# Kernel tuning notes

Measured on AMD Instinct MI355X. Metric: run time of the kernel, lower is better.

The kernel has to match this reference:

```python
import jax, jax.numpy as jnp
import numpy as np

B, S, S2, H, NH, DF, NL, NLAYER = 512, 6, 32, 256, 8, 2048, 3, 3
HD = H // NH


def _layernorm(x, g, b, eps=1e-5):
    mu = x.mean(-1, keepdims=True)
    var = ((x - mu) ** 2).mean(-1, keepdims=True)
    return (x - mu) / jnp.sqrt(var + eps) * g + b


def _pos_encoding(seq, d):
    pos = jnp.arange(seq, dtype=jnp.float32)[:, None]
    div = jnp.exp(jnp.arange(0, d, 2, dtype=jnp.float32) * (-jnp.log(10000.0) / d))
    ang = pos * div  # [seq, d/2]
    return jnp.stack([jnp.sin(ang), jnp.cos(ang)], axis=-1).reshape(seq, d)


def setup_inputs() -> dict:
    key = jax.random.key(0)
    ks = iter(jax.random.split(key, 40))
    sc = 0.02
    inp = {}
    inp['states'] = jax.random.normal(next(ks), (B, S, H), jnp.float32)
    inp['state_mask'] = jax.random.randint(next(ks), (B, S), 0, 2).astype(jnp.float32)
    inp['actions'] = jax.random.normal(next(ks), (B, S2, H), jnp.float32)
    inp['actions_mask'] = jnp.ones((B, S2), jnp.float32)
    # TransformerEncoder params (3 layers, stacked on leading axis)
    inp['Wqkv'] = jax.random.normal(next(ks), (NLAYER, 3 * H, H), jnp.float32) * sc
    inp['bqkv'] = jnp.zeros((NLAYER, 3 * H), jnp.float32)
    inp['Wo'] = jax.random.normal(next(ks), (NLAYER, H, H), jnp.float32) * sc
    inp['bo'] = jnp.zeros((NLAYER, H), jnp.float32)
    inp['ln1_g'] = jnp.ones((NLAYER, H), jnp.float32)
    inp['ln1_b'] = jnp.zeros((NLAYER, H), jnp.float32)
    inp['W1'] = jax.random.normal(next(ks), (NLAYER, DF, H), jnp.float32) * sc
    inp['b1'] = jnp.zeros((NLAYER, DF), jnp.float32)
    inp['W2'] = jax.random.normal(next(ks), (NLAYER, H, DF), jnp.float32) * sc
    inp['b2'] = jnp.zeros((NLAYER, H), jnp.float32)
    inp['ln2_g'] = jnp.ones((NLAYER, H), jnp.float32)
    inp['ln2_b'] = jnp.zeros((NLAYER, H), jnp.float32)
    # attn_layer MLP: Linear(2H->H), ReLU, Linear(H->1), ReLU
    inp['Wa1'] = jax.random.normal(next(ks), (H, 2 * H), jnp.float32) * sc
    inp['ba1'] = jnp.zeros((H,), jnp.float32)
    inp['Wa2'] = jax.random.normal(next(ks), (1, H), jnp.float32) * sc
    inp['ba2'] = jnp.zeros((1,), jnp.float32)
    # dueling value head
    inp['Wv'] = jax.random.normal(next(ks), (1, H), jnp.float32) * sc
    inp['bv'] = jnp.zeros((1,), jnp.float32)
    # per-label bilinear weight [num_labels, H, H] + bias
    inp['Wlab'] = jax.random.normal(next(ks), (NL, H, H), jnp.float32) * sc
    inp['blab'] = jax.random.normal(next(ks), (NL,), jnp.float32) * sc
    return inp


def _forward(states, state_mask, actions, actions_mask, Wqkv, bqkv, Wo, bo,
             ln1_g, ln1_b, W1, b1, W2, b2, ln2_g, ln2_b,
             Wa1, ba1, Wa2, ba2, Wv, bv, Wlab, blab):
    batch, seq, hs = states.shape
    seq2 = actions.shape[1]
    # positional encoding along seq axis (eval mode: dropout = identity)
    x = states + _pos_encoding(seq, hs)[None, :, :]
    # Faithful to original: [batch, seq, h] is fed to a seq-first torch
    # TransformerEncoder, so self-attention mixes across the BATCH axis (L=batch,
    # N=seq). Post-LN layers, relu FFN, dim_feedforward=2048.
    for i in range(NLAYER):
        L, N = x.shape[0], x.shape[1]
        qkv = jnp.einsum('lne,fe->lnf', x, Wqkv[i]) + bqkv[i]
        q, k, v = jnp.split(qkv, 3, axis=-1)
        q = q.reshape(L, N, NH, HD)
        k = k.reshape(L, N, NH, HD)
        v = v.reshape(L, N, NH, HD)
        scores = jnp.einsum('lnhd,mnhd->nhlm', q, k) / jnp.sqrt(jnp.float32(HD))
        attn = jax.nn.softmax(scores, axis=-1)
        ctx = jnp.einsum('nhlm,mnhd->lnhd', attn, v).reshape(L, N, hs)
        sa = jnp.einsum('lne,fe->lnf', ctx, Wo[i]) + bo[i]
        x = _layernorm(x + sa, ln1_g[i], ln1_b[i])
        hmid = jax.nn.relu(jnp.einsum('lne,fe->lnf', x, W1[i]) + b1[i])
        ff = jnp.einsum('lnf,ef->lne', hmid, W2[i]) + b2[i]
        x = _layernorm(x + ff, ln2_g[i], ln2_b[i])
    out = x  # [batch, seq, h]
    # --- attention_aggregate(actions, out, out, actions_mask, state_mask) ---
    mask = actions_mask[:, :, None] * state_mask[:, None, :]  # [B, seq2, seq]
    stack = jnp.concatenate([
        jnp.broadcast_to(actions[:, :, None, :], (batch, seq2, seq, hs)),
        jnp.broadcast_to(out[:, None, :, :], (batch, seq2, seq, hs)),
    ], axis=-1)  # [B, seq2, seq, 2H]
    h1 = jax.nn.relu(jnp.einsum('bqkf,hf->bqkh', stack, Wa1) + ba1)
    a = jax.nn.relu(jnp.einsum('bqkh,oh->bqko', h1, Wa2)[..., 0] + ba2[0])
    A = jnp.where(mask > 0, jnp.exp(a), 0.0)  # masked_fill(-inf).exp()
    attn_w = A / jnp.clip(A.sum(-1, keepdims=True), 2e-15, None)
    states_feat = jnp.einsum('bqk,bkh->bqh', attn_w, out)  # [B, seq2, H]
    # -------------------------------------------------------------------
    actions_num = actions_mask.sum(1)[:, None, None]  # [B,1,1]
    states_feat_mean = states_feat.sum(1, keepdims=True) / actions_num  # [B,1,H]
    # adv[b,s,l] = sum_ij actions[b,s,i] * Wlab[l,i,j] * states_feat[b,s,j] + blab[l]
    adv = jnp.einsum('bsi,lij,bsj->bsl', actions, Wlab, states_feat) + blab
    val = states_feat_mean @ Wv.T + bv  # [B,1,1]
    q_value = val + adv - adv.mean(axis=(1, 2), keepdims=True)  # [B, seq2, NL]
    # actions_mask is all-ones -> no_pad selection keeps every row
    return q_value.reshape(-1, NL)


def reference(states, state_mask, actions, actions_mask, Wqkv, bqkv, Wo, bo,
              ln1_g, ln1_b, W1, b1, W2, b2, ln2_g, ln2_b,
              Wa1, ba1, Wa2, ba2, Wv, bv, Wlab, blab):
    return _forward(states, state_mask, actions, actions_mask, Wqkv, bqkv, Wo, bo,
                    ln1_g, ln1_b, W1, b1, W2, b2, ln2_g, ln2_b,
                    Wa1, ba1, Wa2, ba2, Wv, bv, Wlab, blab)
```

## Files before the change

kernel.cpp:

```cpp
#include <hip/hip_runtime.h>

using u16 = unsigned short;
typedef __attribute__((ext_vector_type(8))) short bf16x8;
typedef __attribute__((ext_vector_type(4))) float f32x4;

__device__ __forceinline__ float b2f(u16 u) { return __uint_as_float(((unsigned)u) << 16); }
__device__ __forceinline__ u16 f2b(float f) {
  unsigned x = __float_as_uint(f);
  return (u16)((x + 0x7FFFu + ((x >> 16) & 1u)) >> 16);
}

__device__ __align__(16) float g_xf[786432];
__device__ __align__(16) u16   g_xb[786432];
__device__ __align__(16) u16   g_qkv[2359296];
__device__ __align__(16) u16   g_ctx[786432];
__device__ __align__(16) u16   g_hmid[6291456];
__device__ __align__(16) u16   g_wb[3932160];
__device__ __align__(16) u16   g_actb[4194304];
__device__ __align__(16) u16   g_wa1b[131072];
__device__ __align__(16) u16   g_wlabb[196608];
__device__ __align__(16) float g_par[344584];
__device__ __align__(16) float g_Pa[4194304];
__device__ __align__(16) float g_Po[786432];
__device__ __align__(16) u16   g_sfb[4194304];
__device__ float g_val[512];
__device__ float g_adv[49152];

#define OFF_BQKV 0
#define OFF_BO   2304
#define OFF_B1   3072
#define OFF_B2   9216
#define OFF_LN1G 9984
#define OFF_LN1B 10752
#define OFF_LN2G 11520
#define OFF_LN2B 12288
#define OFF_BA1  144128
#define OFF_WA2  144384
#define OFF_WV   144640
#define OFF_BLAB 341504
#define OFF_BA2  341508
#define OFF_BV   341509
#define OFF_MASK 341512

#define LP 40

__device__ __forceinline__ int get_flag(const unsigned* ln1g) {
  return (ln1g[0] == 0x3F800000u) ? 0 : 1;
}

struct PJob { const void* src; void* dst; void* dst2; int n; int kind; };
struct PJobs { PJob e[23]; };
__global__ __launch_bounds__(256) void prep_kernel(PJobs jobs, const unsigned* __restrict__ ln1g) {
  PJob j = jobs.e[blockIdx.y];
  int fl = get_flag(ln1g);
  int stride = gridDim.x * 256;
  int i0 = blockIdx.x * 256 + threadIdx.x;
  if (j.kind == 0) {
    float* dst = (float*)j.dst;
    for (int i = i0; i < j.n; i += stride)
      dst[i] = fl ? b2f(((const u16*)j.src)[i]) : ((const float*)j.src)[i];
  } else if (j.kind == 1) {
    int n8 = j.n >> 3;
    uint4* d = (uint4*)j.dst;
    if (fl) {
      const uint4* s = (const uint4*)j.src;
      for (int i = i0; i < n8; i += stride) d[i] = s[i];
    } else {
      const f32x4* s = (const f32x4*)j.src;
      for (int i = i0; i < n8; i += stride) {
        f32x4 v0 = s[i * 2];
        f32x4 v1 = s[i * 2 + 1];
        u16 tmp[8];
        #pragma unroll
        for (int k = 0; k < 4; k++) { tmp[k] = f2b(v0[k]); tmp[4 + k] = f2b(v1[k]); }
        d[i] = *(const uint4*)tmp;
      }
    }
  } else {
    float* xf = (float*)j.dst;
    u16* xb = (u16*)j.dst2;
    const float c = -9.210340371976184f / 256.f;
    for (int i = i0; i < j.n; i += stride) {
      size_t base = (size_t)i * 4;
      int t = (int)(base >> 8);
      int e = (int)(base & 255);
      int n = t % 6;
      int half = e >> 1;
      float dv0 = expf((float)(2 * half) * c);
      float dv1 = expf((float)(2 * (half + 1)) * c);
      float a0 = (float)n * dv0, a1 = (float)n * dv1;
      f32x4 p = { sinf(a0), cosf(a0), sinf(a1), cosf(a1) };
      f32x4 s;
      if (fl) {
        ushort4 u = *(const ushort4*)((const u16*)j.src + base);
        s[0] = b2f(u.x); s[1] = b2f(u.y); s[2] = b2f(u.z); s[3] = b2f(u.w);
      } else {
        s = *(const f32x4*)((const float*)j.src + base);
      }
      f32x4 v;
      #pragma unroll
      for (int k = 0; k < 4; k++) v[k] = s[k] + p[k];
      *(f32x4*)(xf + base) = v;
      ushort4 ob = { f2b(v[0]), f2b(v[1]), f2b(v[2]), f2b(v[3]) };
      *(ushort4*)(xb + base) = ob;
    }
  }
}

__device__ __forceinline__ float block_sum(float v, float* red) {
  int lane = threadIdx.x & 63;
  int w = threadIdx.x >> 6;
  #pragma unroll
  for (int o = 32; o > 0; o >>= 1) v += __shfl_down(v, o, 64);
  __syncthreads();
  if (lane == 0) red[w] = v;
  __syncthreads();
  int nw = blockDim.x >> 6;
  float s = 0.f;
  for (int i = 0; i < nw; i++) s += red[i];
  return s;
}

template <typename TC, bool RELU>
__global__ __launch_bounds__(256) void mfma_gemm(const u16* __restrict__ A,
                                                 const u16* __restrict__ B,
                                                 const float* __restrict__ bias,
                                                 TC* __restrict__ C,
                                                 int K, int lda, int ldb, int ldc) {
  __shared__ __align__(16) short As[64 * LP];
  __shared__ __align__(16) short Bs[64 * LP];
  int tx = threadIdx.x;
  int row0 = blockIdx.y * 64, col0 = blockIdx.x * 64;
  int lr = tx >> 2, lc = (tx & 3) * 8;
  int lane = tx & 63, w = tx >> 6;
  int wr = (w >> 1) * 32, wc = (w & 1) * 32;
  int q = lane >> 4, mr = lane & 15;
  f32x4 acc[2][2] = {};
  const short* Ap = (const short*)A;
  const short* Bp = (const short*)B;
  for (int k0 = 0; k0 < K; k0 += 32) {
    uint4 av = *(const uint4*)(Ap + (size_t)(row0 + lr) * lda + k0 + lc);
    uint4 bv = *(const uint4*)(Bp + (size_t)(col0 + lr) * ldb + k0 + lc);
    __syncthreads();
    *(uint4*)(As + lr * LP + lc) = av;
    *(uint4*)(Bs + lr * LP + lc) = bv;
    __syncthreads();
    bf16x8 af0 = *(const bf16x8*)(As + (wr + mr) * LP + q * 8);
    bf16x8 af1 = *(const bf16x8*)(As + (wr + 16 + mr) * LP + q * 8);
    bf16x8 bf0 = *(const bf16x8*)(Bs + (wc + mr) * LP + q * 8);
    bf16x8 bf1 = *(const bf16x8*)(Bs + (wc + 16 + mr) * LP + q * 8);
    acc[0][0] = __builtin_amdgcn_mfma_f32_16x16x32_bf16(af0, bf0, acc[0][0], 0, 0, 0);
    acc[0][1] = __builtin_amdgcn_mfma_f32_16x16x32_bf16(af0, bf1, acc[0][1], 0, 0, 0);
    acc[1][0] = __builtin_amdgcn_mfma_f32_16x16x32_bf16(af1, bf0, acc[1][0], 0, 0, 0);
    acc[1][1] = __builtin_amdgcn_mfma_f32_16x16x32_bf16(af1, bf1, acc[1][1], 0, 0, 0);
  }
  #pragma unroll
  for (int j = 0; j < 2; j++) {
    int col = col0 + wc + j * 16 + mr;
    float bv_ = bias ? bias[col] : 0.f;
    #pragma unroll
    for (int i = 0; i < 2; i++) {
      #pragma unroll
      for (int r = 0; r < 4; r++) {
        int row = row0 + wr + i * 16 + q * 4 + r;
        float v = acc[i][j][r] + bv_;
        if (RELU) v = fmaxf(v, 0.f);
        if constexpr (sizeof(TC) == 4) C[(size_t)row * ldc + col] = v;
        else C[(size_t)row * ldc + col] = f2b(v);
      }
    }
  }
}

template <typename TC, bool RELU>
__global__ __launch_bounds__(256) void mfma_gemm128(const u16* __restrict__ A,
                                                    const u16* __restrict__ B,
                                                    const float* __restrict__ bias,
                                                    TC* __restrict__ C,
                                                    int K, int lda, int ldb, int ldc) {
  __shared__ __align__(16) short As[128 * LP];
  __shared__ __align__(16) short Bs[128 * LP];
  int tx = threadIdx.x;
  int row0 = blockIdx.y * 128, col0 = blockIdx.x * 128;
  int lr = tx >> 2, lc = (tx & 3) * 8;
  int lane = tx & 63, w = tx >> 6;
  int wr = (w >> 1) * 64, wc = (w & 1) * 64;
  int q = lane >> 4, mr = lane & 15;
  f32x4 acc[4][4] = {};
  const short* Ap = (const short*)A;
  const short* Bp = (const short*)B;
  for (int k0 = 0; k0 < K; k0 += 32) {
    uint4 a0 = *(const uint4*)(Ap + (size_t)(row0 + lr) * lda + k0 + lc);
    uint4 a1 = *(const uint4*)(Ap + (size_t)(row0 + 64 + lr) * lda + k0 + lc);
    uint4 b0 = *(const uint4*)(Bp + (size_t)(col0 + lr) * ldb + k0 + lc);
    uint4 b1 = *(const uint4*)(Bp + (size_t)(col0 + 64 + lr) * ldb + k0 + lc);
    __syncthreads();
    *(uint4*)(As + lr * LP + lc) = a0;
    *(uint4*)(As + (64 + lr) * LP + lc) = a1;
    *(uint4*)(Bs + lr * LP + lc) = b0;
    *(uint4*)(Bs + (64 + lr) * LP + lc) = b1;
    __syncthreads();
    bf16x8 af[4], bf[4];
    #pragma unroll
    for (int i = 0; i < 4; i++) af[i] = *(const bf16x8*)(As + (wr + i * 16 + mr) * LP + q * 8);
    #pragma unroll
    for (int j = 0; j < 4; j++) bf[j] = *(const bf16x8*)(Bs + (wc + j * 16 + mr) * LP + q * 8);
    #pragma unroll
    for (int i = 0; i < 4; i++)
      #pragma unroll
      for (int j = 0; j < 4; j++)
        acc[i][j] = __builtin_amdgcn_mfma_f32_16x16x32_bf16(af[i], bf[j], acc[i][j], 0, 0, 0);
  }
  #pragma unroll
  for (int j = 0; j < 4; j++) {
    int col = col0 + wc + j * 16 + mr;
    float bv_ = bias ? bias[col] : 0.f;
    #pragma unroll
    for (int i = 0; i < 4; i++) {
      #pragma unroll
      for (int r = 0; r < 4; r++) {
        int row = row0 + wr + i * 16 + q * 4 + r;
        float v = acc[i][j][r] + bv_;
        if (RELU) v = fmaxf(v, 0.f);
        if constexpr (sizeof(TC) == 4) C[(size_t)row * ldc + col] = v;
        else C[(size_t)row * ldc + col] = f2b(v);
      }
    }
  }
}

__global__ __launch_bounds__(256) void mfma_gemm_adv(const u16* __restrict__ A,
                                                     const u16* __restrict__ B,
                                                     const u16* __restrict__ actb,
                                                     float* __restrict__ adv,
                                                     int K, int lda, int ldb) {
  __shared__ __align__(16) short As[128 * LP];
  __shared__ __align__(16) short Bs[128 * LP];
  int tx = threadIdx.x;
  int row0 = blockIdx.y * 128, col0 = blockIdx.x * 128;
  int lr = tx >> 2, lc = (tx & 3) * 8;
  int lane = tx & 63, w = tx >> 6;
  int wr = (w >> 1) * 64, wc = (w & 1) * 64;
  int q = lane >> 4, mr = lane & 15;
  f32x4 acc[4][4] = {};
  const short* Ap = (const short*)A;
  const short* Bp = (const short*)B;
  for (int k0 = 0; k0 < K; k0 += 32) {
    uint4 a0 = *(const uint4*)(Ap + (size_t)(row0 + lr) * lda + k0 + lc);
    uint4 a1 = *(const uint4*)(Ap + (size_t)(row0 + 64 + lr) * lda + k0 + lc);
    uint4 b0 = *(const uint4*)(Bp + (size_t)(col0 + lr) * ldb + k0 + lc);
    uint4 b1 = *(const uint4*)(Bp + (size_t)(col0 + 64 + lr) * ldb + k0 + lc);
    __syncthreads();
    *(uint4*)(As + lr * LP + lc) = a0;
    *(uint4*)(As + (64 + lr) * LP + lc) = a1;
    *(uint4*)(Bs + lr * LP + lc) = b0;
    *(uint4*)(Bs + (64 + lr) * LP + lc) = b1;
    __syncthreads();
    bf16x8 af[4], bf[4];
    #pragma unroll
    for (int i = 0; i < 4; i++) af[i] = *(const bf16x8*)(As + (wr + i * 16 + mr) * LP + q * 8);
    #pragma unroll
    for (int j = 0; j < 4; j++) bf[j] = *(const bf16x8*)(Bs + (wc + j * 16 + mr) * LP + q * 8);
    #pragma unroll
    for (int i = 0; i < 4; i++)
      #pragma unroll
      for (int j = 0; j < 4; j++)
        acc[i][j] = __builtin_amdgcn_mfma_f32_16x16x32_bf16(af[i], bf[j], acc[i][j], 0, 0, 0);
  }
  int l = (col0 + wc) >> 8;
  #pragma unroll
  for (int i = 0; i < 4; i++) {
    #pragma unroll
    for (int r = 0; r < 4; r++) {
      int row = row0 + wr + i * 16 + q * 4 + r;
      float s = 0.f;
      #pragma unroll
      for (int j = 0; j < 4; j++) {
        int icol = (col0 + wc + j * 16 + mr) & 255;
        s += acc[i][j][r] * b2f(actb[(size_t)row * 256 + icol]);
      }
      s += __shfl_xor(s, 1, 64);
      s += __shfl_xor(s, 2, 64);
      s += __shfl_xor(s, 4, 64);
      s += __shfl_xor(s, 8, 64);
      if (mr == 0) atomicAdd(&adv[(size_t)row * 3 + l], s);
    }
  }
}

#define LP64 72
template <typename TC, bool RELU>
__global__ __launch_bounds__(256) void mfma_gemm_bk64(const u16* __restrict__ A,
                                                      const u16* __restrict__ B,
                                                      const float* __restrict__ bias,
                                                      TC* __restrict__ C,
                                                      int K, int lda, int ldb, int ldc) {
  __shared__ __align__(16) short As[64 * LP64];
  __shared__ __align__(16) short Bs[64 * LP64];
  int tx = threadIdx.x;
  int row0 = blockIdx.y * 64, col0 = blockIdx.x * 64;
  int lr = tx >> 2, lc = (tx & 3) * 16;
  int lane = tx & 63, w = tx >> 6;
  int wr = (w >> 1) * 32, wc = (w & 1) * 32;
  int q = lane >> 4, mr = lane & 15;
  f32x4 acc[2][2] = {};
  const short* Ap = (const short*)A;
  const short* Bp = (const short*)B;
  for (int k0 = 0; k0 < K; k0 += 64) {
    uint4 a0 = *(const uint4*)(Ap + (size_t)(row0 + lr) * lda + k0 + lc);
    uint4 a1 = *(const uint4*)(Ap + (size_t)(row0 + lr) * lda + k0 + lc + 8);
    uint4 b0 = *(const uint4*)(Bp + (size_t)(col0 + lr) * ldb + k0 + lc);
    uint4 b1 = *(const uint4*)(Bp + (size_t)(col0 + lr) * ldb + k0 + lc + 8);
    __syncthreads();
    *(uint4*)(As + lr * LP64 + lc) = a0;
    *(uint4*)(As + lr * LP64 + lc + 8) = a1;
    *(uint4*)(Bs + lr * LP64 + lc) = b0;
    *(uint4*)(Bs + lr * LP64 + lc + 8) = b1;
    __syncthreads();
    #pragma unroll
    for (int kk = 0; kk < 64; kk += 32) {
      bf16x8 af0 = *(const bf16x8*)(As + (wr + mr) * LP64 + kk + q * 8);
      bf16x8 af1 = *(const bf16x8*)(As + (wr + 16 + mr) * LP64 + kk + q * 8);
      bf16x8 bf0 = *(const bf16x8*)(Bs + (wc + mr) * LP64 + kk + q * 8);
      bf16x8 bf1 = *(const bf16x8*)(Bs + (wc + 16 + mr) * LP64 + kk + q * 8);
      acc[0][0] = __builtin_amdgcn_mfma_f32_16x16x32_bf16(af0, bf0, acc[0][0], 0, 0, 0);
      acc[0][1] = __builtin_amdgcn_mfma_f32_16x16x32_bf16(af0, bf1, acc[0][1], 0, 0, 0);
      acc[1][0] = __builtin_amdgcn_mfma_f32_16x16x32_bf16(af1, bf0, acc[1][0], 0, 0, 0);
      acc[1][1] = __builtin_amdgcn_mfma_f32_16x16x32_bf16(af1, bf1, acc[1][1], 0, 0, 0);
    }
  }
  #pragma unroll
  for (int j = 0; j < 2; j++) {
    int col = col0 + wc + j * 16 + mr;
    float bv_ = bias ? bias[col] : 0.f;
    #pragma unroll
    for (int i = 0; i < 2; i++) {
      #pragma unroll
      for (int r = 0; r < 4; r++) {
        int row = row0 + wr + i * 16 + q * 4 + r;
        float v = acc[i][j][r] + bv_;
        if (RELU) v = fmaxf(v, 0.f);
        if constexpr (sizeof(TC) == 4) C[(size_t)row * ldc + col] = v;
        else C[(size_t)row * ldc + col] = f2b(v);
      }
    }
  }
}

__global__ __launch_bounds__(256) void attn_mfma(const u16* __restrict__ qkv,
                                                 u16* __restrict__ ctx) {
  __shared__ __align__(16) u16 VT[32 * 72];
  __shared__ __align__(16) u16 Ss[64 * 72];
  int tx = threadIdx.x;
  int w = tx >> 6, lane = tx & 63;
  int q = lane >> 4, mr = lane & 15;
  int nh = blockIdx.y;
  int n = nh >> 3, h = nh & 7;
  int l0 = blockIdx.x * 64;
  int lrow = l0 + w * 16 + mr;
  bf16x8 af = *(const bf16x8*)(qkv + ((size_t)lrow * 6 + n) * 768 + h * 32 + q * 8);
  const float scale = 0.17677669529663687f;
  f32x4 acc_o[2] = {};
  float dpart[4] = {0.f, 0.f, 0.f, 0.f};
  for (int mi = 0; mi < 8; mi++) {
    int m0 = mi * 64;
    __syncthreads();
    {
      int row = tx >> 2;
      int dc = (tx & 3) * 8;
      uint4 vv = *(const uint4*)(qkv + ((size_t)(m0 + row) * 6 + n) * 768 + 512 + h * 32 + dc);
      u16 tmp[8];
      *(uint4*)tmp = vv;
      #pragma unroll
      for (int i = 0; i < 8; i++) VT[(dc + i) * 72 + row] = tmp[i];
    }
    f32x4 accs[4];
    #pragma unroll
    for (int nt = 0; nt < 4; nt++) {
      bf16x8 bf = *(const bf16x8*)(qkv + ((size_t)(m0 + nt * 16 + mr) * 6 + n) * 768 +
                                   256 + h * 32 + q * 8);
      f32x4 z = {0.f, 0.f, 0.f, 0.f};
      accs[nt] = __builtin_amdgcn_mfma_f32_16x16x32_bf16(af, bf, z, 0, 0, 0);
    }
    #pragma unroll
    for (int nt = 0; nt < 4; nt++) {
      #pragma unroll
      for (int r = 0; r < 4; r++) {
        float e = __expf(fminf(accs[nt][r] * scale, 60.f));
        dpart[r] += e;
        Ss[(w * 16 + q * 4 + r) * 72 + nt * 16 + mr] = f2b(e);
      }
    }
    __syncthreads();
    #pragma unroll
    for (int dt = 0; dt < 2; dt++) {
      #pragma unroll
      for (int kc = 0; kc < 2; kc++) {
        bf16x8 ap = *(const bf16x8*)(Ss + (w * 16 + mr) * 72 + kc * 32 + q * 8);
        bf16x8 bv = *(const bf16x8*)(VT + (dt * 16 + mr) * 72 + kc * 32 + q * 8);
        acc_o[dt] = __builtin_amdgcn_mfma_f32_16x16x32_bf16(ap, bv, acc_o[dt], 0, 0, 0);
      }
    }
  }
  #pragma unroll
  for (int r = 0; r < 4; r++) {
    float d = dpart[r];
    d += __shfl_xor(d, 1, 64);
    d += __shfl_xor(d, 2, 64);
    d += __shfl_xor(d, 4, 64);
    d += __shfl_xor(d, 8, 64);
    dpart[r] = d;
  }
  #pragma unroll
  for (int dt = 0; dt < 2; dt++) {
    #pragma unroll
    for (int r = 0; r < 4; r++) {
      int l = l0 + w * 16 + q * 4 + r;
      int d = dt * 16 + mr;
      ctx[((size_t)l * 6 + n) * 256 + h * 32 + d] = f2b(acc_o[dt][r] / dpart[r]);
    }
  }
}

__global__ __launch_bounds__(256) void ln_kernel(float* __restrict__ xf,
                                                 u16* __restrict__ xb,
                                                 const u16* __restrict__ addend,
                                                 const float* __restrict__ g,
                                                 const float* __restrict__ b) {
  int row = blockIdx.x * 4 + (threadIdx.x >> 6);
  int lane = threadIdx.x & 63;
  size_t base = (size_t)row * 256 + lane * 4;
  f32x4 x = *(const f32x4*)(xf + base);
  ushort4 ad = *(const ushort4*)(addend + base);
  f32x4 v;
  v[0] = x[0] + b2f(ad.x); v[1] = x[1] + b2f(ad.y);
  v[2] = x[2] + b2f(ad.z); v[3] = x[3] + b2f(ad.w);
  float s = (v[0] + v[1]) + (v[2] + v[3]);
  #pragma unroll
  for (int o = 32; o > 0; o >>= 1) s += __shfl_xor(s, o, 64);
  float mu = s * (1.f / 256.f);
  f32x4 d;
  #pragma unroll
  for (int j = 0; j < 4; j++) d[j] = v[j] - mu;
  float s2 = (d[0] * d[0] + d[1] * d[1]) + (d[2] * d[2] + d[3] * d[3]);
  #pragma unroll
  for (int o = 32; o > 0; o >>= 1) s2 += __shfl_xor(s2, o, 64);
  float rstd = 1.f / sqrtf(s2 * (1.f / 256.f) + 1e-5f);
  f32x4 gg = *(const f32x4*)(g + lane * 4);
  f32x4 bb = *(const f32x4*)(b + lane * 4);
  f32x4 y;
  #pragma unroll
  for (int j = 0; j < 4; j++) y[j] = d[j] * rstd * gg[j] + bb[j];
  *(f32x4*)(xf + base) = y;
  ushort4 ob = { f2b(y[0]), f2b(y[1]), f2b(y[2]), f2b(y[3]) };
  *(ushort4*)(xb + base) = ob;
}

#define PAP 260
__global__ __launch_bounds__(256) void agg_val_kernel(const float* __restrict__ Pa,
                                                      const float* __restrict__ Po,
                                                      const float* __restrict__ Wa2,
                                                      const float* __restrict__ ba2,
                                                      const float* __restrict__ state_mask,
                                                      const float* __restrict__ out,
                                                      const float* __restrict__ Wv,
                                                      const float* __restrict__ bv,
                                                      u16* __restrict__ sfb,
                                                      float* __restrict__ val,
                                                      float* __restrict__ adv) {
  __shared__ __align__(16) float Pa_s[32 * PAP];
  __shared__ __align__(16) float Po_s[6 * PAP];
  __shared__ __align__(16) float out_s[6 * 256];
  __shared__ __align__(16) float wa2_s[256];
  __shared__ float Aw_s[192];
  __shared__ float inv_den_s[32];
  __shared__ float red[4];
  int b = blockIdx.x;
  int tx = threadIdx.x;
  if (tx < 96) adv[(size_t)b * 96 + tx] = 0.f;
  #pragma unroll
  for (int i = tx; i < 2048; i += 256) {
    int r = i >> 6, c4 = (i & 63) * 4;
    f32x4 v = *(const f32x4*)(Pa + ((size_t)(b * 32 + r) * 256 + c4));
    *(f32x4*)(Pa_s + r * PAP + c4) = v;
  }
  if (tx < 128) {
    int r = tx >> 6, c4 = (tx & 63) * 4;
    f32x4 v0 = *(const f32x4*)(Po + ((size_t)(b * 6 + r) * 256 + c4));
    f32x4 v1 = *(const f32x4*)(Po + ((size_t)(b * 6 + r + 2) * 256 + c4));
    f32x4 v2 = *(const f32x4*)(Po + ((size_t)(b * 6 + r + 4) * 256 + c4));
    *(f32x4*)(Po_s + r * PAP + c4) = v0;
    *(f32x4*)(Po_s + (r + 2) * PAP + c4) = v1;
    *(f32x4*)(Po_s + (r + 4) * PAP + c4) = v2;
  } else {
    int i = tx - 128;
    #pragma unroll
    for (int j = 0; j < 3; j++) {
      int e4 = (i + j * 128) * 4;
      f32x4 v = *(const f32x4*)(out + (size_t)b * 1536 + e4);
      *(f32x4*)(out_s + e4) = v;
    }
  }
  if (tx < 64) *(f32x4*)(wa2_s + tx * 4) = *(const f32x4*)(Wa2 + tx * 4);
  __syncthreads();
  if (tx < 192) {
    int q = tx / 6, k = tx - q * 6;
    const float* paP = Pa_s + q * PAP;
    const float* poP = Po_s + k * PAP;
    float a0 = 0.f, a1 = 0.f, a2 = 0.f, a3 = 0.f;
    #pragma unroll 4
    for (int h = 0; h < 256; h += 4) {
      f32x4 pa = *(const f32x4*)(paP + h);
      f32x4 po = *(const f32x4*)(poP + h);
      f32x4 wv = *(const f32x4*)(wa2_s + h);
      a0 += fmaxf(pa[0] + po[0], 0.f) * wv[0];
      a1 += fmaxf(pa[1] + po[1], 0.f) * wv[1];
      a2 += fmaxf(pa[2] + po[2], 0.f) * wv[2];
      a3 += fmaxf(pa[3] + po[3], 0.f) * wv[3];
    }
    float s = (a0 + a1) + (a2 + a3) + ba2[0];
    float a = fminf(fmaxf(s, 0.f), 80.f);
    Aw_s[tx] = (state_mask[b * 6 + k] > 0.f) ? __expf(a) : 0.f;
  }
  __syncthreads();
  if (tx < 32) {
    const float* aw = Aw_s + tx * 6;
    float d = ((aw[0] + aw[1]) + (aw[2] + aw[3])) + (aw[4] + aw[5]);
    inv_den_s[tx] = 1.f / fmaxf(d, 2e-15f);
  }
  __syncthreads();
  float o0 = out_s[tx], o1 = out_s[256 + tx], o2 = out_s[512 + tx];
  float o3 = out_s[768 + tx], o4 = out_s[1024 + tx], o5 = out_s[1280 + tx];
  float msum = 0.f;
  #pragma unroll 4
  for (int q = 0; q < 32; q++) {
    const float* aw = Aw_s + q * 6;
    float acc = aw[0] * o0 + aw[1] * o1 + aw[2] * o2 + aw[3] * o3 + aw[4] * o4 + aw[5] * o5;
    float sfv = acc * inv_den_s[q];
    sfb[((size_t)(b * 32 + q)) * 256 + tx] = f2b(sfv);
    msum += sfv;
  }
  float vc = msum * (1.f / 32.f) * Wv[tx];
  float tot = block_sum(vc, red);
  if (tx == 0) val[b] = tot + bv[0];
}

__global__ __launch_bounds__(128) void final_kernel(const float* __restrict__ adv,
                                                    const float* __restrict__ blab,
                                                    const float* __restrict__ val,
                                                    void* __restrict__ out,
                                                    const unsigned* __restrict__ ln1g) {
  int b = blockIdx.x, t = threadIdx.x;
  __shared__ float red[2];
  float v = (t < 96) ? adv[(size_t)b * 96 + t] + blab[t % 3] : 0.f;
  float s = block_sum(v, red);
  float mean = s * (1.f / 96.f);
  if (t < 96) {
    float q = val[b] + v - mean;
    if (get_flag(ln1g)) ((u16*)out)[(size_t)b * 96 + t] = f2b(q);
    else                ((float*)out)[(size_t)b * 96 + t] = q;
  }
}

extern "C" void kernel_launch(void* const* d_in, const int* in_sizes, int n_in,
                              void* d_out, int out_size, void* d_ws, size_t ws_size,
                              hipStream_t stream) {
  float *xf, *par, *Pa, *Po, *val, *adv;
  u16 *xb, *qkvb, *ctxb, *hmidb, *wb, *actb, *wa1b, *wlabb, *sfb;
  hipGetSymbolAddress((void**)&xf,    HIP_SYMBOL(g_xf));
  hipGetSymbolAddress((void**)&xb,    HIP_SYMBOL(g_xb));
  hipGetSymbolAddress((void**)&qkvb,  HIP_SYMBOL(g_qkv));
  hipGetSymbolAddress((void**)&ctxb,  HIP_SYMBOL(g_ctx));
  hipGetSymbolAddress((void**)&hmidb, HIP_SYMBOL(g_hmid));
  hipGetSymbolAddress((void**)&wb,    HIP_SYMBOL(g_wb));
  hipGetSymbolAddress((void**)&actb,  HIP_SYMBOL(g_actb));
  hipGetSymbolAddress((void**)&wa1b,  HIP_SYMBOL(g_wa1b));
  hipGetSymbolAddress((void**)&wlabb, HIP_SYMBOL(g_wlabb));
  hipGetSymbolAddress((void**)&par,   HIP_SYMBOL(g_par));
  hipGetSymbolAddress((void**)&Pa,    HIP_SYMBOL(g_Pa));
  hipGetSymbolAddress((void**)&Po,    HIP_SYMBOL(g_Po));
  hipGetSymbolAddress((void**)&sfb,   HIP_SYMBOL(g_sfb));
  hipGetSymbolAddress((void**)&val,   HIP_SYMBOL(g_val));
  hipGetSymbolAddress((void**)&adv,   HIP_SYMBOL(g_adv));
  const unsigned* ln1g = (const unsigned*)d_in[8];
  u16* sab = hmidb;
  u16* ffb = ctxb;

  PJobs pj;
  pj.e[0]  = { d_in[5],  par + OFF_BQKV, nullptr, 2304, 0 };
  pj.e[1]  = { d_in[7],  par + OFF_BO,   nullptr, 768,  0 };
  pj.e[2]  = { d_in[11], par + OFF_B1,   nullptr, 6144, 0 };
  pj.e[3]  = { d_in[13], par + OFF_B2,   nullptr, 768,  0 };
  pj.e[4]  = { d_in[8],  par + OFF_LN1G, nullptr, 768,  0 };
  pj.e[5]  = { d_in[9],  par + OFF_LN1B, nullptr, 768,  0 };
  pj.e[6]  = { d_in[14], par + OFF_LN2G, nullptr, 768,  0 };
  pj.e[7]  = { d_in[15], par + OFF_LN2B, nullptr, 768,  0 };
  pj.e[8]  = { d_in[17], par + OFF_BA1,  nullptr, 256,  0 };
  pj.e[9]  = { d_in[18], par + OFF_WA2,  nullptr, 256,  0 };
  pj.e[10] = { d_in[20], par + OFF_WV,   nullptr, 256,  0 };
  pj.e[11] = { d_in[23], par + OFF_BLAB, nullptr, 3,    0 };
  pj.e[12] = { d_in[19], par + OFF_BA2,  nullptr, 1,    0 };
  pj.e[13] = { d_in[21], par + OFF_BV,   nullptr, 1,    0 };
  pj.e[14] = { d_in[1],  par + OFF_MASK, nullptr, 3072, 0 };
  pj.e[15] = { d_in[4],  wb,             nullptr, 589824,  1 };
  pj.e[16] = { d_in[6],  wb + 589824,    nullptr, 196608,  1 };
  pj.e[17] = { d_in[10], wb + 786432,    nullptr, 1572864, 1 };
  pj.e[18] = { d_in[12], wb + 2359296,   nullptr, 1572864, 1 };
  pj.e[19] = { d_in[16], wa1b,           nullptr, 131072,  1 };
  pj.e[20] = { d_in[22], wlabb,          nullptr, 196608,  1 };
  pj.e[21] = { d_in[2],  actb,           nullptr, 4194304, 1 };
  pj.e[22] = { d_in[0],  xf,             xb,      196608,  2 };
  prep_kernel<<<dim3(128, 23), 256, 0, stream>>>(pj, ln1g);

  for (int i = 0; i < 3; i++) {
    mfma_gemm128<u16, false><<<dim3(6, 24), 256, 0, stream>>>(
        xb, wb + (size_t)i * 196608, par + OFF_BQKV + i * 768, qkvb, 256, 256, 256, 768);
    attn_mfma<<<dim3(8, 48), 256, 0, stream>>>(qkvb, ctxb);
    mfma_gemm<u16, false><<<dim3(4, 48), 256, 0, stream>>>(
        ctxb, wb + 589824 + (size_t)i * 65536, par + OFF_BO + i * 256, sab, 256, 256, 256, 256);
    ln_kernel<<<768, 256, 0, stream>>>(xf, xb, sab, par + OFF_LN1G + i * 256, par + OFF_LN1B + i * 256);
    mfma_gemm128<u16, true><<<dim3(16, 24), 256, 0, stream>>>(
        xb, wb + 786432 + (size_t)i * 524288, par + OFF_B1 + i * 2048, hmidb, 256, 256, 256, 2048);
    mfma_gemm_bk64<u16, false><<<dim3(4, 48), 256, 0, stream>>>(
        hmidb, wb + 2359296 + (size_t)i * 524288, par + OFF_B2 + i * 256, ffb, 2048, 2048, 2048, 256);
    ln_kernel<<<768, 256, 0, stream>>>(xf, xb, ffb, par + OFF_LN2G + i * 256, par + OFF_LN2B + i * 256);
  }

  mfma_gemm128<float, false><<<dim3(2, 128), 256, 0, stream>>>(
      actb, wa1b, par + OFF_BA1, Pa, 256, 256, 512, 256);
  mfma_gemm<float, false><<<dim3(4, 48), 256, 0, stream>>>(
      xb, wa1b + 256, nullptr, Po, 256, 256, 512, 256);

  agg_val_kernel<<<512, 256, 0, stream>>>(Pa, Po, par + OFF_WA2, par + OFF_BA2,
                                          par + OFF_MASK, xf, par + OFF_WV,
                                          par + OFF_BV, sfb, val, adv);

  mfma_gemm_adv<<<dim3(6, 128), 256, 0, stream>>>(sfb, wlabb, actb, adv, 256, 256, 256);
  final_kernel<<<512, 128, 0, stream>>>(adv, par + OFF_BLAB, val, d_out, ln1g);
}
```

Baseline: 286.9 us.

## Store attention MLP projections in bf16, fuse Pa/Po GEMMs, retile QKV and W2 GEMMs

Merges the two attention-MLP projection GEMMs into a single launch and stores their outputs as bf16 instead of fp32, halving intermediate traffic into agg_val_kernel. Replaces the W2 GEMM with a 64x32 output tile so twice as many blocks run in parallel, and moves the QKV projection from the 128-tile GEMM to the smaller-tile GEMM for more blocks. The bf16 storage of Pa/Po adds rounding before the ReLU/attention-score stage, which slightly changes numerics.

```diff
diff --git a/kernel.cpp b/kernel.cpp
--- a/kernel.cpp
+++ b/kernel.cpp
@@ -20,8 +20,8 @@
 __device__ __align__(16) u16   g_wa1b[131072];
 __device__ __align__(16) u16   g_wlabb[196608];
 __device__ __align__(16) float g_par[344584];
-__device__ __align__(16) float g_Pa[4194304];
-__device__ __align__(16) float g_Po[786432];
+__device__ __align__(16) u16   g_Pab[4194304];
+__device__ __align__(16) u16   g_Pob[786432];
 __device__ __align__(16) u16   g_sfb[4194304];
 __device__ float g_val[512];
 __device__ float g_adv[49152];
@@ -229,6 +229,71 @@
   }
 }
 
+__global__ __launch_bounds__(256) void papo_kernel(const u16* __restrict__ actb,
+                                                   const u16* __restrict__ xb,
+                                                   const u16* __restrict__ wa1b,
+                                                   const float* __restrict__ ba1,
+                                                   u16* __restrict__ Pab,
+                                                   u16* __restrict__ Pob) {
+  __shared__ __align__(16) short As[128 * LP];
+  __shared__ __align__(16) short Bs[128 * LP];
+  const short* Ap;
+  const short* Bp;
+  const float* bias;
+  u16* C;
+  int row0;
+  if (blockIdx.y < 128) {
+    Ap = (const short*)actb; Bp = (const short*)wa1b; bias = ba1; C = Pab;
+    row0 = blockIdx.y * 128;
+  } else {
+    Ap = (const short*)xb; Bp = (const short*)(wa1b + 256); bias = nullptr; C = Pob;
+    row0 = (blockIdx.y - 128) * 128;
+  }
+  const int K = 256, lda = 256, ldb = 512, ldc = 256;
+  int tx = threadIdx.x;
+  int col0 = blockIdx.x * 128;
+  int lr = tx >> 2, lc = (tx & 3) * 8;
+  int lane = tx & 63, w = tx >> 6;
+  int wr = (w >> 1) * 64, wc = (w & 1) * 64;
+  int q = lane >> 4, mr = lane & 15;
+  f32x4 acc[4][4] = {};
+  for (int k0 = 0; k0 < K; k0 += 32) {
+    uint4 a0 = *(const uint4*)(Ap + (size_t)(row0 + lr) * lda + k0 + lc);
+    uint4 a1 = *(const uint4*)(Ap + (size_t)(row0 + 64 + lr) * lda + k0 + lc);
+    uint4 b0 = *(const uint4*)(Bp + (size_t)(col0 + lr) * ldb + k0 + lc);
+    uint4 b1 = *(const uint4*)(Bp + (size_t)(col0 + 64 + lr) * ldb + k0 + lc);
+    __syncthreads();
+    *(uint4*)(As + lr * LP + lc) = a0;
+    *(uint4*)(As + (64 + lr) * LP + lc) = a1;
+    *(uint4*)(Bs + lr * LP + lc) = b0;
+    *(uint4*)(Bs + (64 + lr) * LP + lc) = b1;
+    __syncthreads();
+    bf16x8 af[4], bf[4];
+    #pragma unroll
+    for (int i = 0; i < 4; i++) af[i] = *(const bf16x8*)(As + (wr + i * 16 + mr) * LP + q * 8);
+    #pragma unroll
+    for (int j = 0; j < 4; j++) bf[j] = *(const bf16x8*)(Bs + (wc + j * 16 + mr) * LP + q * 8);
+    #pragma unroll
+    for (int i = 0; i < 4; i++)
+      #pragma unroll
+      for (int j = 0; j < 4; j++)
+        acc[i][j] = __builtin_amdgcn_mfma_f32_16x16x32_bf16(af[i], bf[j], acc[i][j], 0, 0, 0);
+  }
+  #pragma unroll
+  for (int j = 0; j < 4; j++) {
+    int col = col0 + wc + j * 16 + mr;
+    float bv_ = bias ? bias[col] : 0.f;
+    #pragma unroll
+    for (int i = 0; i < 4; i++) {
+      #pragma unroll
+      for (int r = 0; r < 4; r++) {
+        int row = row0 + wr + i * 16 + q * 4 + r;
+        C[(size_t)row * ldc + col] = f2b(acc[i][j][r] + bv_);
+      }
+    }
+  }
+}
+
 __global__ __launch_bounds__(256) void mfma_gemm_adv(const u16* __restrict__ A,
                                                      const u16* __restrict__ B,
                                                      const u16* __restrict__ actb,
@@ -289,60 +354,49 @@
 }
 
 #define LP64 72
-template <typename TC, bool RELU>
-__global__ __launch_bounds__(256) void mfma_gemm_bk64(const u16* __restrict__ A,
-                                                      const u16* __restrict__ B,
-                                                      const float* __restrict__ bias,
-                                                      TC* __restrict__ C,
-                                                      int K, int lda, int ldb, int ldc) {
+__global__ __launch_bounds__(256) void mfma_gemm_w2(const u16* __restrict__ A,
+                                                    const u16* __restrict__ B,
+                                                    const float* __restrict__ bias,
+                                                    u16* __restrict__ C,
+                                                    int K, int lda, int ldb, int ldc) {
   __shared__ __align__(16) short As[64 * LP64];
-  __shared__ __align__(16) short Bs[64 * LP64];
+  __shared__ __align__(16) short Bs[32 * LP64];
   int tx = threadIdx.x;
-  int row0 = blockIdx.y * 64, col0 = blockIdx.x * 64;
-  int lr = tx >> 2, lc = (tx & 3) * 16;
+  int row0 = blockIdx.y * 64, col0 = blockIdx.x * 32;
   int lane = tx & 63, w = tx >> 6;
-  int wr = (w >> 1) * 32, wc = (w & 1) * 32;
+  int wr = (w >> 1) * 32, wc = (w & 1) * 16;
   int q = lane >> 4, mr = lane & 15;
-  f32x4 acc[2][2] = {};
+  int alr = tx >> 2, alc = (tx & 3) * 16;
+  int blr = tx >> 3, blc = (tx & 7) * 8;
+  f32x4 acc[2] = {};
   const short* Ap = (const short*)A;
   const short* Bp = (const short*)B;
   for (int k0 = 0; k0 < K; k0 += 64) {
-    uint4 a0 = *(const uint4*)(Ap + (size_t)(row0 + lr) * lda + k0 + lc);
-    uint4 a1 = *(const uint4*)(Ap + (size_t)(row0 + lr) * lda + k0 + lc + 8);
-    uint4 b0 = *(const uint4*)(Bp + (size_t)(col0 + lr) * ldb + k0 + lc);
-    uint4 b1 = *(const uint4*)(Bp + (size_t)(col0 + lr) * ldb + k0 + lc + 8);
-    __syncthreads();
-    *(uint4*)(As + lr * LP64 + lc) = a0;
-    *(uint4*)(As + lr * LP64 + lc + 8) = a1;
-    *(uint4*)(Bs + lr * LP64 + lc) = b0;
-    *(uint4*)(Bs + lr * LP64 + lc + 8) = b1;
+    uint4 a0 = *(const uint4*)(Ap + (size_t)(row0 + alr) * lda + k0 + alc);
+    uint4 a1 = *(const uint4*)(Ap + (size_t)(row0 + alr) * lda + k0 + alc + 8);
+    uint4 b0 = *(const uint4*)(Bp + (size_t)(col0 + blr) * ldb + k0 + blc);
+    __syncthreads();
+    *(uint4*)(As + alr * LP64 + alc) = a0;
+    *(uint4*)(As + alr * LP64 + alc + 8) = a1;
+    *(uint4*)(Bs + blr * LP64 + blc) = b0;
     __syncthreads();
     #pragma unroll
     for (int kk = 0; kk < 64; kk += 32) {
       bf16x8 af0 = *(const bf16x8*)(As + (wr + mr) * LP64 + kk + q * 8);
       bf16x8 af1 = *(const bf16x8*)(As + (wr + 16 + mr) * LP64 + kk + q * 8);
-      bf16x8 bf0 = *(const bf16x8*)(Bs + (wc + mr) * LP64 + kk + q * 8);
-      bf16x8 bf1 = *(const bf16x8*)(Bs + (wc + 16 + mr) * LP64 + kk + q * 8);
-      acc[0][0] = __builtin_amdgcn_mfma_f32_16x16x32_bf16(af0, bf0, acc[0][0], 0, 0, 0);
-      acc[0][1] = __builtin_amdgcn_mfma_f32_16x16x32_bf16(af0, bf1, acc[0][1], 0, 0, 0);
-      acc[1][0] = __builtin_amdgcn_mfma_f32_16x16x32_bf16(af1, bf0, acc[1][0], 0, 0, 0);
-      acc[1][1] = __builtin_amdgcn_mfma_f32_16x16x32_bf16(af1, bf1, acc[1][1], 0, 0, 0);
-    }
-  }
-  #pragma unroll
-  for (int j = 0; j < 2; j++) {
-    int col = col0 + wc + j * 16 + mr;
-    float bv_ = bias ? bias[col] : 0.f;
-    #pragma unroll
-    for (int i = 0; i < 2; i++) {
-      #pragma unroll
-      for (int r = 0; r < 4; r++) {
-        int row = row0 + wr + i * 16 + q * 4 + r;
-        float v = acc[i][j][r] + bv_;
-        if (RELU) v = fmaxf(v, 0.f);
-        if constexpr (sizeof(TC) == 4) C[(size_t)row * ldc + col] = v;
-        else C[(size_t)row * ldc + col] = f2b(v);
-      }
+      bf16x8 bf = *(const bf16x8*)(Bs + (wc + mr) * LP64 + kk + q * 8);
+      acc[0] = __builtin_amdgcn_mfma_f32_16x16x32_bf16(af0, bf, acc[0], 0, 0, 0);
+      acc[1] = __builtin_amdgcn_mfma_f32_16x16x32_bf16(af1, bf, acc[1], 0, 0, 0);
+    }
+  }
+  int col = col0 + wc + mr;
+  float bv_ = bias ? bias[col] : 0.f;
+  #pragma unroll
+  for (int i = 0; i < 2; i++) {
+    #pragma unroll
+    for (int r = 0; r < 4; r++) {
+      int row = row0 + wr + i * 16 + q * 4 + r;
+      C[(size_t)row * ldc + col] = f2b(acc[i][r] + bv_);
     }
   }
 }
@@ -457,8 +511,8 @@
 }
 
 #define PAP 260
-__global__ __launch_bounds__(256) void agg_val_kernel(const float* __restrict__ Pa,
-                                                      const float* __restrict__ Po,
+__global__ __launch_bounds__(256) void agg_val_kernel(const u16* __restrict__ Pab,
+                                                      const u16* __restrict__ Pob,
                                                       const float* __restrict__ Wa2,
                                                       const float* __restrict__ ba2,
                                                       const float* __restrict__ state_mask,
@@ -479,27 +533,23 @@
   int tx = threadIdx.x;
   if (tx < 96) adv[(size_t)b * 96 + tx] = 0.f;
   #pragma unroll
-  for (int i = tx; i < 2048; i += 256) {
-    int r = i >> 6, c4 = (i & 63) * 4;
-    f32x4 v = *(const f32x4*)(Pa + ((size_t)(b * 32 + r) * 256 + c4));
-    *(f32x4*)(Pa_s + r * PAP + c4) = v;
-  }
-  if (tx < 128) {
-    int r = tx >> 6, c4 = (tx & 63) * 4;
-    f32x4 v0 = *(const f32x4*)(Po + ((size_t)(b * 6 + r) * 256 + c4));
-    f32x4 v1 = *(const f32x4*)(Po + ((size_t)(b * 6 + r + 2) * 256 + c4));
-    f32x4 v2 = *(const f32x4*)(Po + ((size_t)(b * 6 + r + 4) * 256 + c4));
-    *(f32x4*)(Po_s + r * PAP + c4) = v0;
-    *(f32x4*)(Po_s + (r + 2) * PAP + c4) = v1;
-    *(f32x4*)(Po_s + (r + 4) * PAP + c4) = v2;
-  } else {
-    int i = tx - 128;
-    #pragma unroll
-    for (int j = 0; j < 3; j++) {
-      int e4 = (i + j * 128) * 4;
-      f32x4 v = *(const f32x4*)(out + (size_t)b * 1536 + e4);
-      *(f32x4*)(out_s + e4) = v;
-    }
+  for (int i = tx; i < 1024; i += 256) {
+    int r = i >> 5, c8 = (i & 31) * 8;
+    u16 vv[8];
+    *(uint4*)vv = *(const uint4*)(Pab + ((size_t)(b * 32 + r) * 256 + c8));
+    #pragma unroll
+    for (int k = 0; k < 8; k++) Pa_s[r * PAP + c8 + k] = b2f(vv[k]);
+  }
+  if (tx < 192) {
+    int r = tx >> 5, c8 = (tx & 31) * 8;
+    u16 vv[8];
+    *(uint4*)vv = *(const uint4*)(Pob + ((size_t)(b * 6 + r) * 256 + c8));
+    #pragma unroll
+    for (int k = 0; k < 8; k++) Po_s[r * PAP + c8 + k] = b2f(vv[k]);
+  }
+  for (int i = tx; i < 384; i += 256) {
+    int e4 = i * 4;
+    *(f32x4*)(out_s + e4) = *(const f32x4*)(out + (size_t)b * 1536 + e4);
   }
   if (tx < 64) *(f32x4*)(wa2_s + tx * 4) = *(const f32x4*)(Wa2 + tx * 4);
   __syncthreads();
@@ -565,8 +615,8 @@
 extern "C" void kernel_launch(void* const* d_in, const int* in_sizes, int n_in,
                               void* d_out, int out_size, void* d_ws, size_t ws_size,
                               hipStream_t stream) {
-  float *xf, *par, *Pa, *Po, *val, *adv;
-  u16 *xb, *qkvb, *ctxb, *hmidb, *wb, *actb, *wa1b, *wlabb, *sfb;
+  float *xf, *par, *val, *adv;
+  u16 *xb, *qkvb, *ctxb, *hmidb, *wb, *actb, *wa1b, *wlabb, *sfb, *Pab, *Pob;
   hipGetSymbolAddress((void**)&xf,    HIP_SYMBOL(g_xf));
   hipGetSymbolAddress((void**)&xb,    HIP_SYMBOL(g_xb));
   hipGetSymbolAddress((void**)&qkvb,  HIP_SYMBOL(g_qkv));
@@ -577,8 +627,8 @@
   hipGetSymbolAddress((void**)&wa1b,  HIP_SYMBOL(g_wa1b));
   hipGetSymbolAddress((void**)&wlabb, HIP_SYMBOL(g_wlabb));
   hipGetSymbolAddress((void**)&par,   HIP_SYMBOL(g_par));
-  hipGetSymbolAddress((void**)&Pa,    HIP_SYMBOL(g_Pa));
-  hipGetSymbolAddress((void**)&Po,    HIP_SYMBOL(g_Po));
+  hipGetSymbolAddress((void**)&Pab,   HIP_SYMBOL(g_Pab));
+  hipGetSymbolAddress((void**)&Pob,   HIP_SYMBOL(g_Pob));
   hipGetSymbolAddress((void**)&sfb,   HIP_SYMBOL(g_sfb));
   hipGetSymbolAddress((void**)&val,   HIP_SYMBOL(g_val));
   hipGetSymbolAddress((void**)&adv,   HIP_SYMBOL(g_adv));
@@ -613,7 +663,7 @@
   prep_kernel<<<dim3(128, 23), 256, 0, stream>>>(pj, ln1g);
 
   for (int i = 0; i < 3; i++) {
-    mfma_gemm128<u16, false><<<dim3(6, 24), 256, 0, stream>>>(
+    mfma_gemm<u16, false><<<dim3(12, 48), 256, 0, stream>>>(
         xb, wb + (size_t)i * 196608, par + OFF_BQKV + i * 768, qkvb, 256, 256, 256, 768);
     attn_mfma<<<dim3(8, 48), 256, 0, stream>>>(qkvb, ctxb);
     mfma_gemm<u16, false><<<dim3(4, 48), 256, 0, stream>>>(
@@ -621,17 +671,14 @@
     ln_kernel<<<768, 256, 0, stream>>>(xf, xb, sab, par + OFF_LN1G + i * 256, par + OFF_LN1B + i * 256);
     mfma_gemm128<u16, true><<<dim3(16, 24), 256, 0, stream>>>(
         xb, wb + 786432 + (size_t)i * 524288, par + OFF_B1 + i * 2048, hmidb, 256, 256, 256, 2048);
-    mfma_gemm_bk64<u16, false><<<dim3(4, 48), 256, 0, stream>>>(
+    mfma_gemm_w2<<<dim3(8, 48), 256, 0, stream>>>(
         hmidb, wb + 2359296 + (size_t)i * 524288, par + OFF_B2 + i * 256, ffb, 2048, 2048, 2048, 256);
     ln_kernel<<<768, 256, 0, stream>>>(xf, xb, ffb, par + OFF_LN2G + i * 256, par + OFF_LN2B + i * 256);
   }
 
-  mfma_gemm128<float, false><<<dim3(2, 128), 256, 0, stream>>>(
-      actb, wa1b, par + OFF_BA1, Pa, 256, 256, 512, 256);
-  mfma_gemm<float, false><<<dim3(4, 48), 256, 0, stream>>>(
-      xb, wa1b + 256, nullptr, Po, 256, 256, 512, 256);
-
-  agg_val_kernel<<<512, 256, 0, stream>>>(Pa, Po, par + OFF_WA2, par + OFF_BA2,
+  papo_kernel<<<dim3(2, 152), 256, 0, stream>>>(actb, xb, wa1b, par + OFF_BA1, Pab, Pob);
+
+  agg_val_kernel<<<512, 256, 0, stream>>>(Pab, Pob, par + OFF_WA2, par + OFF_BA2,
                                           par + OFF_MASK, xf, par + OFF_WV,
                                           par + OFF_BV, sfb, val, adv);
 
```

After: 266.1 us. 1.08x faster.
